# Kernel tuning notes

Measured on AMD Instinct MI355X. Metric: run time of the kernel, lower is better.

The kernel has to match this reference:

```python
import jax, jax.numpy as jnp
import numpy as np

N_NODES = 100000
N_EDGES = 3200000
FEAT = 16


def gcn_conv(x, src, dst, W, b):
    # PyG GCNConv: add self-loops, symmetric normalization deg^{-1/2}(A+I)deg^{-1/2},
    # then linear transform and scatter-add aggregation.
    n = x.shape[0]
    loop = jnp.arange(n, dtype=src.dtype)
    s = jnp.concatenate([src, loop])
    d = jnp.concatenate([dst, loop])
    deg = jax.ops.segment_sum(jnp.ones_like(d, dtype=x.dtype), d, num_segments=n)
    dinv = jnp.where(deg > 0, jax.lax.rsqrt(deg), 0.0)
    norm = dinv[s] * dinv[d]  # [E+N]
    h = x @ W  # [N, out]
    msg = h[s] * norm[:, None]  # gather + weight
    out = jax.ops.segment_sum(msg, d, num_segments=n)  # scatter-add
    return out + b


def setup_inputs() -> dict:
    key = jax.random.key(0)
    k1, k2, k3, k4 = jax.random.split(key, 4)
    scale = 1.0 / np.sqrt(FEAT)
    return {
        "x": jax.random.normal(k1, (N_NODES, FEAT), dtype=jnp.float32),
        "edge_index": jax.random.randint(k2, (2, N_EDGES), 0, N_NODES, dtype=jnp.int64) if jax.config.jax_enable_x64 else jax.random.randint(k2, (2, N_EDGES), 0, N_NODES, dtype=jnp.int32),
        "W1": jax.random.normal(k3, (FEAT, 16), dtype=jnp.float32) * scale,
        "b1": jnp.zeros((16,), dtype=jnp.float32),
        "W2": jax.random.normal(k4, (16, FEAT), dtype=jnp.float32) * scale,
        "b2": jnp.zeros((FEAT,), dtype=jnp.float32),
    }


def reference(x, edge_index, W1, b1, W2, b2):
    src, dst = edge_index[0], edge_index[1]
    h = gcn_conv(x, src, dst, W1, b1)
    h = jax.nn.relu(h)
    out = gcn_conv(h, src, dst, W2, b2)
    return out
```

## Files before the change

### kernel.cpp

```cpp
#include <hip/hip_runtime.h>

#define F 16
#define BSHIFT 8
#define NPB 256
#define NB 391
#define CH 4096
#define BCAP 9216


__global__ void init_cursor_kernel(unsigned* __restrict__ cursor) {
    int i = threadIdx.x;
    if (i < NB) cursor[i * 16] = (unsigned)(i * BCAP);
}

__global__ __launch_bounds__(512) void
reorder_kernel(const int* __restrict__ src, const int* __restrict__ dst,
               unsigned* __restrict__ cursor, unsigned* __restrict__ recs, int E) {
    __shared__ unsigned lsorted[CH];
    __shared__ unsigned short lbkt[CH];
    __shared__ unsigned cnt[NB];
    __shared__ unsigned lstart[NB + 1];
    int t = threadIdx.x, b = blockIdx.x;
    int e0 = b * CH;
    int cnt_e = E - e0; if (cnt_e > CH) cnt_e = CH;

    for (int i = t; i < NB; i += 512) cnt[i] = 0;
    __syncthreads();
    unsigned pk[8];
#pragma unroll
    for (int j = 0; j < 8; ++j) {
        int i = t + j * 512;
        pk[j] = 0xFFFFFFFFu;
        if (i < cnt_e) {
            unsigned d = (unsigned)dst[e0 + i];
            unsigned bk = d >> BSHIFT;
            unsigned r = atomicAdd(&cnt[bk], 1u);
            pk[j] = bk | ((d & 255u) << 9) | (r << 17);
        }
    }
    __syncthreads();
    if (t < 64) {
        unsigned run = 0;
        for (int c = 0; c < NB; c += 64) {
            int idx = c + t;
            unsigned v = (idx < NB) ? cnt[idx] : 0u;
            unsigned inc = v;
#pragma unroll
            for (int d = 1; d < 64; d <<= 1) {
                unsigned o = __shfl_up(inc, d, 64);
                if (t >= d) inc += o;
            }
            if (idx < NB) lstart[idx] = run + inc - v;
            run += __shfl(inc, 63, 64);
        }
        if (t == 0) lstart[NB] = (unsigned)cnt_e;
    }
    __syncthreads();
    for (int i = t; i < NB; i += 512) {
        unsigned c = cnt[i];
        if (c) cnt[i] = atomicAdd(&cursor[i * 16], c);
    }
    __syncthreads();
#pragma unroll
    for (int j = 0; j < 8; ++j) {
        int i = t + j * 512;
        if (i < cnt_e) {
            unsigned p = pk[j];
            unsigned bk = p & 0x1FFu;
            unsigned low = (p >> 9) & 255u;
            unsigned r = p >> 17;
            unsigned pos = lstart[bk] + r;
            lsorted[pos] = (unsigned)src[e0 + i] | (low << 17);
            lbkt[pos] = (unsigned short)bk;
        }
    }
    __syncthreads();
    for (int i = t; i < cnt_e; i += 512) {
        unsigned bk = lbkt[i];
        recs[cnt[bk] + ((unsigned)i - lstart[bk])] = lsorted[i];
    }
}

__global__ __launch_bounds__(1024) void
sort2_kernel(const unsigned* __restrict__ recs, const unsigned* __restrict__ cursor,
             unsigned* __restrict__ srcs, int* __restrict__ noff, int* __restrict__ nend,
             float* __restrict__ dinv, int n) {
    __shared__ unsigned lsort[BCAP];
    __shared__ unsigned cnt[NPB];
    __shared__ unsigned ex[NPB];
    __shared__ unsigned wtot[4];
    int t = threadIdx.x, b = blockIdx.x;
    int e0 = b * BCAP;
    int used = (int)(cursor[b * 16] - (unsigned)e0);
    if (t < NPB) cnt[t] = 0;
    __syncthreads();
    unsigned pk[9];
#pragma unroll
    for (int j = 0; j < 9; ++j) {
        int i = t + j * 1024;
        pk[j] = 0xFFFFFFFFu;
        if (i < used) {
            unsigned node = recs[e0 + i] >> 17;
            unsigned r = atomicAdd(&cnt[node], 1u);
            pk[j] = node | (r << 8);
        }
    }
    __syncthreads();
    if (t < NPB) {
        unsigned c = cnt[t];
        unsigned inc = c;
        int lane = t & 63, w = t >> 6;
#pragma unroll
        for (int d = 1; d < 64; d <<= 1) {
            unsigned o = __shfl_up(inc, d, 64);
            if (lane >= d) inc += o;
        }
        if (lane == 63) wtot[w] = inc;
        __syncthreads();
        unsigned wbase = 0;
        for (int i = 0; i < w; ++i) wbase += wtot[i];
        unsigned e = wbase + inc - c;
        ex[t] = e;
        int node = b * NPB + t;
        if (node < n) {
            noff[node] = e0 + (int)e;
            nend[node] = e0 + (int)(e + c);
            dinv[node] = rsqrtf((float)c + 1.0f);
        }
    } else {
        __syncthreads();
    }
    __syncthreads();
#pragma unroll
    for (int j = 0; j < 9; ++j) {
        int i = t + j * 1024;
        if (i < used) {
            unsigned p = pk[j];
            lsort[ex[p & 255u] + (p >> 8)] = recs[e0 + i] & 0x1FFFFu;
        }
    }
    __syncthreads();
    for (int i = t; i < used; i += 1024) srcs[e0 + i] = lsort[i];
}

__global__ void linear_kernel(const float* __restrict__ in, const float* __restrict__ dinv,
                              const float* __restrict__ W, float* __restrict__ out, int n) {
    __shared__ float Ws[F * F];
    __shared__ float As[64][F + 1];
    int t = threadIdx.x;
    Ws[t] = W[t];
    int g = t >> 2, c = t & 3;
    int node = blockIdx.x * 64 + g;
    float4 v = {0.f, 0.f, 0.f, 0.f};
    if (node < n) v = ((const float4*)in)[(size_t)node * 4 + c];
    As[g][c * 4 + 0] = v.x; As[g][c * 4 + 1] = v.y;
    As[g][c * 4 + 2] = v.z; As[g][c * 4 + 3] = v.w;
    __syncthreads();
    if (node < n) {
        float di = dinv[node];
        float4 o = {0.f, 0.f, 0.f, 0.f};
        int j = c * 4;
#pragma unroll
        for (int k = 0; k < F; ++k) {
            float ak = As[g][k];
            o.x += ak * Ws[k * F + j + 0];
            o.y += ak * Ws[k * F + j + 1];
            o.z += ak * Ws[k * F + j + 2];
            o.w += ak * Ws[k * F + j + 3];
        }
        o.x *= di; o.y *= di; o.z *= di; o.w *= di;
        ((float4*)out)[(size_t)node * 4 + c] = o;
    }
}

__global__ void agg_csr_kernel(const float* __restrict__ hin, const unsigned* __restrict__ srcs,
                               const int* __restrict__ noff, const int* __restrict__ nend,
                               const float* __restrict__ dinv,
                               const float* __restrict__ Wn, const float* __restrict__ bias,
                               float* __restrict__ outp, int n, int mode) {
    __shared__ float a1[64][F + 1];
    __shared__ float Ws[F * F];
    int t = threadIdx.x;
    int g = t >> 2, c = t & 3;
    if (mode == 1) Ws[t] = Wn[t];
    int node = blockIdx.x * 64 + g;
    const float4* h4 = (const float4*)hin;
    float4 val = {0.f, 0.f, 0.f, 0.f};
    float di = 0.f;
    if (node < n) {
        di = dinv[node];
        int e0 = noff[node], e1 = nend[node];
        float4 s0 = {0,0,0,0}, s1 = {0,0,0,0}, s2 = {0,0,0,0}, s3 = {0,0,0,0};
        int e = e0;
        for (; e + 4 <= e1; e += 4) {
            int ia = srcs[e], ib = srcs[e + 1], ic = srcs[e + 2], id = srcs[e + 3];
            float4 va = h4[(size_t)ia * 4 + c];
            float4 vb = h4[(size_t)ib * 4 + c];
            float4 vc = h4[(size_t)ic * 4 + c];
            float4 vd = h4[(size_t)id * 4 + c];
            s0.x += va.x; s0.y += va.y; s0.z += va.z; s0.w += va.w;
            s1.x += vb.x; s1.y += vb.y; s1.z += vb.z; s1.w += vb.w;
            s2.x += vc.x; s2.y += vc.y; s2.z += vc.z; s2.w += vc.w;
            s3.x += vd.x; s3.y += vd.y; s3.z += vd.z; s3.w += vd.w;
        }
        for (; e < e1; ++e) {
            float4 va = h4[(size_t)srcs[e] * 4 + c];
            s0.x += va.x; s0.y += va.y; s0.z += va.z; s0.w += va.w;
        }
        float4 self = h4[(size_t)node * 4 + c];
        float4 bi = ((const float4*)bias)[c];
        val.x = di * ((s0.x + s1.x) + (s2.x + s3.x) + self.x) + bi.x;
        val.y = di * ((s0.y + s1.y) + (s2.y + s3.y) + self.y) + bi.y;
        val.z = di * ((s0.z + s1.z) + (s2.z + s3.z) + self.z) + bi.z;
        val.w = di * ((s0.w + s1.w) + (s2.w + s3.w) + self.w) + bi.w;
        if (mode == 1) {
            val.x = fmaxf(val.x, 0.f); val.y = fmaxf(val.y, 0.f);
            val.z = fmaxf(val.z, 0.f); val.w = fmaxf(val.w, 0.f);
        }
    }
    if (mode == 1) {
        a1[g][c * 4 + 0] = val.x; a1[g][c * 4 + 1] = val.y;
        a1[g][c * 4 + 2] = val.z; a1[g][c * 4 + 3] = val.w;
        __syncthreads();
        if (node < n) {
            float4 o = {0.f, 0.f, 0.f, 0.f};
            int j = c * 4;
#pragma unroll
            for (int k = 0; k < F; ++k) {
                float ak = a1[g][k];
                o.x += ak * Ws[k * F + j + 0];
                o.y += ak * Ws[k * F + j + 1];
                o.z += ak * Ws[k * F + j + 2];
                o.w += ak * Ws[k * F + j + 3];
            }
            o.x *= di; o.y *= di; o.z *= di; o.w *= di;
            ((float4*)outp)[(size_t)node * 4 + c] = o;
        }
    } else {
        if (node < n) ((float4*)outp)[(size_t)node * 4 + c] = val;
    }
}


__global__ void deg_kernel(const int* __restrict__ dst, float* __restrict__ deg, int E) {
    int e = blockIdx.x * blockDim.x + threadIdx.x;
    if (e < E) atomicAdd(&deg[dst[e]], 1.0f);
}
__global__ void dinv_kernel(float* __restrict__ deg, int n) {
    int i = blockIdx.x * blockDim.x + threadIdx.x;
    if (i < n) deg[i] = rsqrtf(deg[i] + 1.0f);
}
__global__ void linear2_kernel(const float* __restrict__ in, const float* __restrict__ acc,
                               const float* __restrict__ dinv, const float* __restrict__ W,
                               const float* __restrict__ bias, float* __restrict__ out,
                               int n, int mode) {
    __shared__ float Ws[F * F];
    __shared__ float As[16][F + 1];
    int t = threadIdx.x;
    Ws[t] = W[t];
    int nb = t >> 4, j = t & 15;
    int i = blockIdx.x * 16 + nb;
    float di = 0.f, v = 0.f;
    if (i < n) {
        di = dinv[i]; v = in[i * F + j];
        if (mode) { v = di * (acc[i * F + j] + v) + bias[j]; v = fmaxf(v, 0.f); }
    }
    As[nb][j] = v;
    __syncthreads();
    if (i < n) {
        float s = 0.f;
#pragma unroll
        for (int k = 0; k < F; ++k) s += As[nb][k] * Ws[k * F + j];
        out[i * F + j] = s * di;
    }
}
__global__ void scatter_kernel(const int* __restrict__ src, const int* __restrict__ dst,
                               const float* __restrict__ h, float* __restrict__ acc, int E) {
    int t = blockIdx.x * blockDim.x + threadIdx.x;
    int e = t >> 4, j = t & 15;
    if (e < E) atomicAdd(&acc[dst[e] * F + j], h[src[e] * F + j]);
}
__global__ void out_kernel(const float* __restrict__ acc, const float* __restrict__ h,
                           const float* __restrict__ dinv, const float* __restrict__ bias,
                           float* __restrict__ out, int n) {
    int t = blockIdx.x * blockDim.x + threadIdx.x;
    if (t < n * F) {
        int i = t >> 4, j = t & 15;
        out[t] = dinv[i] * (acc[t] + h[t]) + bias[j];
    }
}


extern "C" void kernel_launch(void* const* d_in, const int* in_sizes, int n_in,
                              void* d_out, int out_size, void* d_ws, size_t ws_size,
                              hipStream_t stream) {
    const float* x  = (const float*)d_in[0];
    const int*   ei = (const int*)d_in[1];
    const float* W1 = (const float*)d_in[2];
    const float* b1 = (const float*)d_in[3];
    const float* W2 = (const float*)d_in[4];
    const float* b2 = (const float*)d_in[5];
    float* outp = (float*)d_out;

    const int N = in_sizes[0] / F;
    const int E = in_sizes[1] / 2;
    const int* src = ei;
    const int* dst = ei + E;

    const int nb_rt = (N + NPB - 1) >> BSHIFT;
    const size_t RC = (size_t)NB * BCAP;
    size_t need = sizeof(unsigned) * ((size_t)N * 19 + 2 * RC + 16 * NB);

    if (nb_rt == NB && E <= CH * 65535 && ws_size >= need) {
        float* dinv = (float*)d_ws;
        float* hA = dinv + N;
        unsigned* recs = (unsigned*)(hA + (size_t)F * N);
        float* hB = (float*)recs;
        unsigned* srcs = recs + RC;
        int* noff = (int*)(srcs + RC);
        int* nend = noff + N;
        unsigned* cursor = (unsigned*)(nend + N);

        init_cursor_kernel<<<1, 512, 0, stream>>>(cursor);
        reorder_kernel<<<(E + CH - 1) / CH, 512, 0, stream>>>(src, dst, cursor, recs, E);
        sort2_kernel<<<NB, 1024, 0, stream>>>(recs, cursor, srcs, noff, nend, dinv, N);
        linear_kernel<<<(N + 63) / 64, 256, 0, stream>>>(x, dinv, W1, hA, N);
        agg_csr_kernel<<<(N + 63) / 64, 256, 0, stream>>>(hA, srcs, noff, nend, dinv, W2, b1, hB, N, 1);
        agg_csr_kernel<<<(N + 63) / 64, 256, 0, stream>>>(hB, srcs, noff, nend, dinv, nullptr, b2, outp, N, 2);
    } else {
        float* dinv = (float*)d_ws;
        float* h = dinv + N;
        float* acc = h + (size_t)F * N;
        hipMemsetAsync(dinv, 0, (size_t)N * sizeof(float), stream);
        hipMemsetAsync(acc, 0, (size_t)F * N * sizeof(float), stream);
        deg_kernel<<<(E + 255) / 256, 256, 0, stream>>>(dst, dinv, E);
        dinv_kernel<<<(N + 255) / 256, 256, 0, stream>>>(dinv, N);
        linear2_kernel<<<(N + 15) / 16, 256, 0, stream>>>(x, nullptr, dinv, W1, nullptr, h, N, 0);
        scatter_kernel<<<((size_t)E * F + 255) / 256, 256, 0, stream>>>(src, dst, h, acc, E);
        linear2_kernel<<<(N + 15) / 16, 256, 0, stream>>>(h, acc, dinv, W2, b1, h, N, 1);
        hipMemsetAsync(acc, 0, (size_t)F * N * sizeof(float), stream);
        scatter_kernel<<<((size_t)E * F + 255) / 256, 256, 0, stream>>>(src, dst, h, acc, E);
        out_kernel<<<((size_t)N * F + 255) / 256, 256, 0, stream>>>(acc, h, dinv, b2, outp, N);
    }
}
```

Before: 214.1 us.

## Aggregate before linear transform and fold dinv scaling into sort kernel

The kernel uses linearity (A·(xW) = (A·x)W) to aggregate raw dinv-scaled features first and apply the 16x16 weight matrix afterward inside each aggregation kernel. The separate linear kernel is removed, and the dinv scaling of x moves into the tail of sort2_kernel. Source and record values are also kept in registers so reorder and sort2 do not reload them from global memory. The intent is one fewer launch and one fewer full pass over node features, at the cost of a small matmul in both aggregation passes and slightly different floating-point rounding.

```diff
diff --git a/kernel.cpp b/kernel.cpp
--- a/kernel.cpp
+++ b/kernel.cpp
@@ -26,13 +26,14 @@
 
     for (int i = t; i < NB; i += 512) cnt[i] = 0;
     __syncthreads();
-    unsigned pk[8];
+    unsigned pk[8], rs[8];
 #pragma unroll
     for (int j = 0; j < 8; ++j) {
         int i = t + j * 512;
         pk[j] = 0xFFFFFFFFu;
         if (i < cnt_e) {
             unsigned d = (unsigned)dst[e0 + i];
+            rs[j] = (unsigned)src[e0 + i];
             unsigned bk = d >> BSHIFT;
             unsigned r = atomicAdd(&cnt[bk], 1u);
             pk[j] = bk | ((d & 255u) << 9) | (r << 17);
@@ -67,10 +68,8 @@
         if (i < cnt_e) {
             unsigned p = pk[j];
             unsigned bk = p & 0x1FFu;
-            unsigned low = (p >> 9) & 255u;
-            unsigned r = p >> 17;
-            unsigned pos = lstart[bk] + r;
-            lsorted[pos] = (unsigned)src[e0 + i] | (low << 17);
+            unsigned pos = lstart[bk] + (p >> 17);
+            lsorted[pos] = rs[j] | (((p >> 9) & 255u) << 17);
             lbkt[pos] = (unsigned short)bk;
         }
     }
@@ -84,23 +83,27 @@
 __global__ __launch_bounds__(1024) void
 sort2_kernel(const unsigned* __restrict__ recs, const unsigned* __restrict__ cursor,
              unsigned* __restrict__ srcs, int* __restrict__ noff, int* __restrict__ nend,
-             float* __restrict__ dinv, int n) {
+             float* __restrict__ dinv, const float* __restrict__ x,
+             float* __restrict__ z, int n) {
     __shared__ unsigned lsort[BCAP];
     __shared__ unsigned cnt[NPB];
     __shared__ unsigned ex[NPB];
+    __shared__ float ldv[NPB];
     __shared__ unsigned wtot[4];
     int t = threadIdx.x, b = blockIdx.x;
     int e0 = b * BCAP;
     int used = (int)(cursor[b * 16] - (unsigned)e0);
     if (t < NPB) cnt[t] = 0;
     __syncthreads();
-    unsigned pk[9];
+    unsigned pk[9], rsr[9];
 #pragma unroll
     for (int j = 0; j < 9; ++j) {
         int i = t + j * 1024;
         pk[j] = 0xFFFFFFFFu;
         if (i < used) {
-            unsigned node = recs[e0 + i] >> 17;
+            unsigned rec = recs[e0 + i];
+            unsigned node = rec >> 17;
+            rsr[j] = rec & 0x1FFFFu;
             unsigned r = atomicAdd(&cnt[node], 1u);
             pk[j] = node | (r << 8);
         }
@@ -121,11 +124,13 @@
         for (int i = 0; i < w; ++i) wbase += wtot[i];
         unsigned e = wbase + inc - c;
         ex[t] = e;
+        float dv = rsqrtf((float)c + 1.0f);
+        ldv[t] = dv;
         int node = b * NPB + t;
         if (node < n) {
             noff[node] = e0 + (int)e;
             nend[node] = e0 + (int)(e + c);
-            dinv[node] = rsqrtf((float)c + 1.0f);
+            dinv[node] = dv;
         }
     } else {
         __syncthreads();
@@ -136,56 +141,34 @@
         int i = t + j * 1024;
         if (i < used) {
             unsigned p = pk[j];
-            lsort[ex[p & 255u] + (p >> 8)] = recs[e0 + i] & 0x1FFFFu;
+            lsort[ex[p & 255u] + (p >> 8)] = rsr[j];
         }
     }
     __syncthreads();
     for (int i = t; i < used; i += 1024) srcs[e0 + i] = lsort[i];
-}
-
-__global__ void linear_kernel(const float* __restrict__ in, const float* __restrict__ dinv,
-                              const float* __restrict__ W, float* __restrict__ out, int n) {
-    __shared__ float Ws[F * F];
-    __shared__ float As[64][F + 1];
-    int t = threadIdx.x;
-    Ws[t] = W[t];
-    int g = t >> 2, c = t & 3;
-    int node = blockIdx.x * 64 + g;
-    float4 v = {0.f, 0.f, 0.f, 0.f};
-    if (node < n) v = ((const float4*)in)[(size_t)node * 4 + c];
-    As[g][c * 4 + 0] = v.x; As[g][c * 4 + 1] = v.y;
-    As[g][c * 4 + 2] = v.z; As[g][c * 4 + 3] = v.w;
-    __syncthreads();
-    if (node < n) {
-        float di = dinv[node];
-        float4 o = {0.f, 0.f, 0.f, 0.f};
-        int j = c * 4;
-#pragma unroll
-        for (int k = 0; k < F; ++k) {
-            float ak = As[g][k];
-            o.x += ak * Ws[k * F + j + 0];
-            o.y += ak * Ws[k * F + j + 1];
-            o.z += ak * Ws[k * F + j + 2];
-            o.w += ak * Ws[k * F + j + 3];
-        }
-        o.x *= di; o.y *= di; o.z *= di; o.w *= di;
-        ((float4*)out)[(size_t)node * 4 + c] = o;
+    {
+        int node = b * NPB + (t >> 2);
+        if (node < n) {
+            float4 v = ((const float4*)x)[(size_t)b * 1024 + t];
+            float dv = ldv[t >> 2];
+            v.x *= dv; v.y *= dv; v.z *= dv; v.w *= dv;
+            ((float4*)z)[(size_t)b * 1024 + t] = v;
+        }
     }
 }
 
 __global__ void agg_csr_kernel(const float* __restrict__ hin, const unsigned* __restrict__ srcs,
                                const int* __restrict__ noff, const int* __restrict__ nend,
                                const float* __restrict__ dinv,
-                               const float* __restrict__ Wn, const float* __restrict__ bias,
+                               const float* __restrict__ W, const float* __restrict__ bias,
                                float* __restrict__ outp, int n, int mode) {
     __shared__ float a1[64][F + 1];
     __shared__ float Ws[F * F];
     int t = threadIdx.x;
     int g = t >> 2, c = t & 3;
-    if (mode == 1) Ws[t] = Wn[t];
+    Ws[t] = W[t];
     int node = blockIdx.x * 64 + g;
     const float4* h4 = (const float4*)hin;
-    float4 val = {0.f, 0.f, 0.f, 0.f};
     float di = 0.f;
     if (node < n) {
         di = dinv[node];
@@ -208,36 +191,31 @@
             s0.x += va.x; s0.y += va.y; s0.z += va.z; s0.w += va.w;
         }
         float4 self = h4[(size_t)node * 4 + c];
+        a1[g][c * 4 + 0] = (s0.x + s1.x) + (s2.x + s3.x) + self.x;
+        a1[g][c * 4 + 1] = (s0.y + s1.y) + (s2.y + s3.y) + self.y;
+        a1[g][c * 4 + 2] = (s0.z + s1.z) + (s2.z + s3.z) + self.z;
+        a1[g][c * 4 + 3] = (s0.w + s1.w) + (s2.w + s3.w) + self.w;
+    }
+    __syncthreads();
+    if (node < n) {
+        float4 o = {0.f, 0.f, 0.f, 0.f};
+        int j = c * 4;
+#pragma unroll
+        for (int k = 0; k < F; ++k) {
+            float ak = a1[g][k];
+            o.x += ak * Ws[k * F + j + 0];
+            o.y += ak * Ws[k * F + j + 1];
+            o.z += ak * Ws[k * F + j + 2];
+            o.w += ak * Ws[k * F + j + 3];
+        }
         float4 bi = ((const float4*)bias)[c];
-        val.x = di * ((s0.x + s1.x) + (s2.x + s3.x) + self.x) + bi.x;
-        val.y = di * ((s0.y + s1.y) + (s2.y + s3.y) + self.y) + bi.y;
-        val.z = di * ((s0.z + s1.z) + (s2.z + s3.z) + self.z) + bi.z;
-        val.w = di * ((s0.w + s1.w) + (s2.w + s3.w) + self.w) + bi.w;
+        o.x = di * o.x + bi.x; o.y = di * o.y + bi.y;
+        o.z = di * o.z + bi.z; o.w = di * o.w + bi.w;
         if (mode == 1) {
-            val.x = fmaxf(val.x, 0.f); val.y = fmaxf(val.y, 0.f);
-            val.z = fmaxf(val.z, 0.f); val.w = fmaxf(val.w, 0.f);
-        }
-    }
-    if (mode == 1) {
-        a1[g][c * 4 + 0] = val.x; a1[g][c * 4 + 1] = val.y;
-        a1[g][c * 4 + 2] = val.z; a1[g][c * 4 + 3] = val.w;
-        __syncthreads();
-        if (node < n) {
-            float4 o = {0.f, 0.f, 0.f, 0.f};
-            int j = c * 4;
-#pragma unroll
-            for (int k = 0; k < F; ++k) {
-                float ak = a1[g][k];
-                o.x += ak * Ws[k * F + j + 0];
-                o.y += ak * Ws[k * F + j + 1];
-                o.z += ak * Ws[k * F + j + 2];
-                o.w += ak * Ws[k * F + j + 3];
-            }
-            o.x *= di; o.y *= di; o.z *= di; o.w *= di;
-            ((float4*)outp)[(size_t)node * 4 + c] = o;
-        }
-    } else {
-        if (node < n) ((float4*)outp)[(size_t)node * 4 + c] = val;
+            o.x = fmaxf(o.x, 0.f) * di; o.y = fmaxf(o.y, 0.f) * di;
+            o.z = fmaxf(o.z, 0.f) * di; o.w = fmaxf(o.w, 0.f) * di;
+        }
+        ((float4*)outp)[(size_t)node * 4 + c] = o;
     }
 }
 
@@ -313,9 +291,9 @@
 
     if (nb_rt == NB && E <= CH * 65535 && ws_size >= need) {
         float* dinv = (float*)d_ws;
-        float* hA = dinv + N;
-        unsigned* recs = (unsigned*)(hA + (size_t)F * N);
-        float* hB = (float*)recs;
+        float* z = dinv + N;
+        unsigned* recs = (unsigned*)(z + (size_t)F * N);
+        float* y = (float*)recs;
         unsigned* srcs = recs + RC;
         int* noff = (int*)(srcs + RC);
         int* nend = noff + N;
@@ -323,10 +301,9 @@
 
         init_cursor_kernel<<<1, 512, 0, stream>>>(cursor);
         reorder_kernel<<<(E + CH - 1) / CH, 512, 0, stream>>>(src, dst, cursor, recs, E);
-        sort2_kernel<<<NB, 1024, 0, stream>>>(recs, cursor, srcs, noff, nend, dinv, N);
-        linear_kernel<<<(N + 63) / 64, 256, 0, stream>>>(x, dinv, W1, hA, N);
-        agg_csr_kernel<<<(N + 63) / 64, 256, 0, stream>>>(hA, srcs, noff, nend, dinv, W2, b1, hB, N, 1);
-        agg_csr_kernel<<<(N + 63) / 64, 256, 0, stream>>>(hB, srcs, noff, nend, dinv, nullptr, b2, outp, N, 2);
+        sort2_kernel<<<NB, 1024, 0, stream>>>(recs, cursor, srcs, noff, nend, dinv, x, z, N);
+        agg_csr_kernel<<<(N + 63) / 64, 256, 0, stream>>>(z, srcs, noff, nend, dinv, W1, b1, y, N, 1);
+        agg_csr_kernel<<<(N + 63) / 64, 256, 0, stream>>>(y, srcs, noff, nend, dinv, W2, b2, outp, N, 2);
     } else {
         float* dinv = (float*)d_ws;
         float* h = dinv + N;
```

After: 206.3 us. 1.04x faster.
